# Kernel optimization log

Hardware: AMD Instinct MI355X
Metric: run time of the kernel (lower is better)

The kernel has to match this reference:

```python
import jax, jax.numpy as jnp
import numpy as np

B, S, D, H = 2, 2048, 1024, 16
DH = D // H


def setup_inputs() -> dict:
    key = jax.random.key(0)
    ks = jax.random.split(key, 12)
    sc = 1.0 / np.sqrt(D)
    return {
        "query": jax.random.normal(ks[0], (B, S, D), jnp.float32),
        "key": jax.random.normal(ks[1], (B, S, D), jnp.float32),
        "value": jax.random.normal(ks[2], (B, S, D), jnp.float32),
        "key_mask": jax.random.randint(ks[3], (B, S), 0, 2, jnp.int32),
        "Wq": jax.random.normal(ks[4], (D, D), jnp.float32) * sc,
        "bq": jnp.zeros((D,), jnp.float32),
        "Wk": jax.random.normal(ks[5], (D, D), jnp.float32) * sc,
        "bk": jnp.zeros((D,), jnp.float32),
        "Wv": jax.random.normal(ks[6], (D, D), jnp.float32) * sc,
        "bv": jnp.zeros((D,), jnp.float32),
        "Wo": jax.random.normal(ks[7], (D, D), jnp.float32) * sc,
        "bo": jnp.zeros((D,), jnp.float32),
    }


def _shape(x):
    # (B, L, D) -> (B, H, L, DH)
    return x.reshape(B, -1, H, DH).transpose(0, 2, 1, 3)


def reference(query, key, value, key_mask, Wq, bq, Wk, bk, Wv, bv, Wo, bo):
    # linear projections (torch Linear: x @ W.T + b)
    q = _shape(query @ Wq.T + bq)  # (B,H,S,DH)
    k = _shape(key @ Wk.T + bk)
    v = _shape(value @ Wv.T + bv)

    q = q / jnp.sqrt(jnp.asarray(DH, q.dtype))
    scores = jnp.einsum("bhqd,bhkd->bhqk", q, k)  # (B,H,S,S)

    pad = (key_mask == 0)[:, None, None, :]  # (B,1,1,K)
    scores = jnp.where(pad, jnp.asarray(-1e18, scores.dtype), scores)
    attn = jax.nn.softmax(scores, axis=-1)
    attn = jnp.where(pad, jnp.asarray(0.0, attn.dtype), attn)
    # dropout p=0.0 (eval) -> identity

    ctx = jnp.einsum("bhqk,bhkd->bhqd", attn, v)
    ctx = ctx.transpose(0, 2, 1, 3).reshape(B, -1, D)  # unshape
    output = ctx @ Wo.T + bo
    return (output, attn)
```

## Files before the change

### kernel.cpp

```cpp
#include <hip/hip_runtime.h>

#define B_  2
#define S_  2048
#define D_  1024
#define H_  16
#define DH_ 64

typedef _Float16 f16;
typedef f16   f16x2 __attribute__((ext_vector_type(2)));
typedef f16   f16x4 __attribute__((ext_vector_type(4)));
typedef f16   f16x8 __attribute__((ext_vector_type(8)));
typedef float f32x4 __attribute__((ext_vector_type(4)));
typedef float f32x16 __attribute__((ext_vector_type(16)));

static __device__ __forceinline__ f16x8 ldsm8(const f16* p) {
    return *reinterpret_cast<const f16x8*>(p);
}

static __device__ __forceinline__ int swz(int row, int byteInRow) {
    return row * 128 + (byteInRow ^ ((row & 7) << 4));
}

static __device__ __forceinline__ void gll16(const void* g, void* l) {
    __builtin_amdgcn_global_load_lds(
        (const __attribute__((address_space(1))) void*)g,
        (__attribute__((address_space(3))) void*)l, 16, 0, 0);
}

static __device__ __forceinline__ unsigned pk16(float a, float b) {
    return __builtin_bit_cast(unsigned, __builtin_amdgcn_cvt_pkrtz(a, b));
}

__global__ __launch_bounds__(256)
void qkv_gemm(const float* __restrict__ Aq, const float* __restrict__ Ak,
              const float* __restrict__ Av,
              const float* __restrict__ Wq, const float* __restrict__ Wk,
              const float* __restrict__ Wv,
              const float* __restrict__ bq, const float* __restrict__ bk,
              const float* __restrict__ bv,
              f16* __restrict__ qo, f16* __restrict__ ko, f16* __restrict__ vo,
              float qscale)
{
    constexpr int K = 1024, N = 1024;
    __shared__ __align__(16) f16 As[128][40];
    __shared__ __align__(16) f16 Bs[128][40];
    const int z = blockIdx.z;
    const float* A    = z == 0 ? Aq : z == 1 ? Ak : Av;
    const float* W    = z == 0 ? Wq : z == 1 ? Wk : Wv;
    const float* bias = z == 0 ? bq : z == 1 ? bk : bv;
    const float scale = z == 0 ? qscale : 1.0f;

    const int t  = threadIdx.x;
    const int bm = blockIdx.y * 128;
    const int bn = blockIdx.x * 128;
    const int w  = t >> 6, l = t & 63;
    const int wr = w >> 1, wc = w & 1;
    const int lr = l & 15, lg = l >> 4;

    f32x4 acc[4][4];
    #pragma unroll
    for (int m = 0; m < 4; ++m)
        #pragma unroll
        for (int n = 0; n < 4; ++n)
            acc[m][n] = (f32x4){0.f, 0.f, 0.f, 0.f};

    for (int kt = 0; kt < K / 32; ++kt) {
        #pragma unroll
        for (int i = 0; i < 4; ++i) {
            int idx = t + i * 256;
            int row = idx >> 3, g = idx & 7;
            float4 v = *reinterpret_cast<const float4*>(A + (size_t)(bm + row) * K + kt * 32 + g * 4);
            alignas(8) f16 hh[4] = {(f16)v.x, (f16)v.y, (f16)v.z, (f16)v.w};
            *reinterpret_cast<uint2*>(&As[row][g * 4]) = *reinterpret_cast<uint2*>(hh);
        }
        #pragma unroll
        for (int i = 0; i < 4; ++i) {
            int idx = t + i * 256;
            int row = idx >> 3, g = idx & 7;
            float4 v = *reinterpret_cast<const float4*>(W + (size_t)(bn + row) * K + kt * 32 + g * 4);
            alignas(8) f16 hh[4] = {(f16)v.x, (f16)v.y, (f16)v.z, (f16)v.w};
            *reinterpret_cast<uint2*>(&Bs[row][g * 4]) = *reinterpret_cast<uint2*>(hh);
        }
        __syncthreads();

        f16x8 af[4], bfv[4];
        #pragma unroll
        for (int m = 0; m < 4; ++m) af[m]  = ldsm8(&As[wr * 64 + m * 16 + lr][lg * 8]);
        #pragma unroll
        for (int n = 0; n < 4; ++n) bfv[n] = ldsm8(&Bs[wc * 64 + n * 16 + lr][lg * 8]);
        #pragma unroll
        for (int m = 0; m < 4; ++m)
            #pragma unroll
            for (int n = 0; n < 4; ++n)
                acc[m][n] = __builtin_amdgcn_mfma_f32_16x16x32_f16(af[m], bfv[n], acc[m][n], 0, 0, 0);
        __syncthreads();
    }

    #pragma unroll
    for (int m = 0; m < 4; ++m) {
        #pragma unroll
        for (int n = 0; n < 4; ++n) {
            int col = bn + wc * 64 + n * 16 + lr;
            float bb = bias[col];
            if (z == 2) {
                int row0 = bm + wr * 64 + m * 16 + lg * 4;
                int b = row0 >> 11, s = row0 & 2047;
                int hh_ = col >> 6, d = col & 63;
                alignas(8) f16 hv[4];
                #pragma unroll
                for (int j = 0; j < 4; ++j)
                    hv[j] = (f16)(acc[m][n][j] + bb);
                *reinterpret_cast<uint2*>(vo +
                    (((size_t)(b * 16 + hh_) * 64 + d) * 2048 + s)) =
                    *reinterpret_cast<uint2*>(hv);
            } else {
                f16* Cp = z == 0 ? qo : ko;
                #pragma unroll
                for (int j = 0; j < 4; ++j) {
                    int row = bm + wr * 64 + m * 16 + lg * 4 + j;
                    Cp[(size_t)row * N + col] = (f16)((acc[m][n][j] + bb) * scale);
                }
            }
        }
    }
}

__global__ __launch_bounds__(256)
void gemm_out(const f16* __restrict__ A, const float* __restrict__ W,
              const float* __restrict__ bias, float* __restrict__ Cp)
{
    constexpr int K = 1024, N = 1024;
    __shared__ __align__(16) f16 As[128][40];
    __shared__ __align__(16) f16 Bs[128][40];
    const int t  = threadIdx.x;
    const int bm = blockIdx.y * 128;
    const int bn = blockIdx.x * 128;
    const int w  = t >> 6, l = t & 63;
    const int wr = w >> 1, wc = w & 1;
    const int lr = l & 15, lg = l >> 4;

    f32x4 acc[4][4];
    #pragma unroll
    for (int m = 0; m < 4; ++m)
        #pragma unroll
        for (int n = 0; n < 4; ++n)
            acc[m][n] = (f32x4){0.f, 0.f, 0.f, 0.f};

    for (int kt = 0; kt < K / 32; ++kt) {
        #pragma unroll
        for (int i = 0; i < 2; ++i) {
            int idx = t + i * 256;
            int row = idx >> 2, g = idx & 3;
            *reinterpret_cast<uint4*>(&As[row][g * 8]) =
                *reinterpret_cast<const uint4*>(A + (size_t)(bm + row) * K + kt * 32 + g * 8);
        }
        #pragma unroll
        for (int i = 0; i < 4; ++i) {
            int idx = t + i * 256;
            int row = idx >> 3, g = idx & 7;
            float4 v = *reinterpret_cast<const float4*>(W + (size_t)(bn + row) * K + kt * 32 + g * 4);
            alignas(8) f16 hh[4] = {(f16)v.x, (f16)v.y, (f16)v.z, (f16)v.w};
            *reinterpret_cast<uint2*>(&Bs[row][g * 4]) = *reinterpret_cast<uint2*>(hh);
        }
        __syncthreads();

        f16x8 af[4], bfv[4];
        #pragma unroll
        for (int m = 0; m < 4; ++m) af[m]  = ldsm8(&As[wr * 64 + m * 16 + lr][lg * 8]);
        #pragma unroll
        for (int n = 0; n < 4; ++n) bfv[n] = ldsm8(&Bs[wc * 64 + n * 16 + lr][lg * 8]);
        #pragma unroll
        for (int m = 0; m < 4; ++m)
            #pragma unroll
            for (int n = 0; n < 4; ++n)
                acc[m][n] = __builtin_amdgcn_mfma_f32_16x16x32_f16(af[m], bfv[n], acc[m][n], 0, 0, 0);
        __syncthreads();
    }

    #pragma unroll
    for (int m = 0; m < 4; ++m) {
        #pragma unroll
        for (int n = 0; n < 4; ++n) {
            int col = bn + wc * 64 + n * 16 + lr;
            float bb = bias[col];
            #pragma unroll
            for (int j = 0; j < 4; ++j) {
                int row = bm + wr * 64 + m * 16 + lg * 4 + j;
                Cp[(size_t)row * N + col] = acc[m][n][j] + bb;
            }
        }
    }
}

__global__ __launch_bounds__(256, 3)
void attn_fused(const f16* __restrict__ qh, const f16* __restrict__ khp,
                const f16* __restrict__ vtg, const int* __restrict__ kmask,
                float* __restrict__ attn_out, f16* __restrict__ ch)
{
    __shared__ __align__(16) f16 ksd[2][64 * 64];
    __shared__ __align__(16) f16 vsd[2][64 * 64];
    __shared__ unsigned mbits[64];

    const int t  = threadIdx.x;
    const int w  = t >> 6, l = t & 63, lo = l & 31, hi = l >> 5;
    const bool H1 = (hi == 1);

    const int bid  = blockIdx.x;
    const int xcd  = bid & 7;
    const int slot = bid >> 3;
    const int bh   = (xcd << 2) | (slot >> 4);
    const int qt   = slot & 15;
    const int b    = bh >> 4;
    const int h    = bh & 15;
    const int q0   = qt * 128;
    const int row  = q0 + w * 32 + lo;

    f16x8 qf[4];
    {
        const f16* qb = qh + (size_t)(b * S_ + row) * D_ + h * DH_ + hi * 8;
        #pragma unroll
        for (int c = 0; c < 4; ++c) qf[c] = *reinterpret_cast<const f16x8*>(qb + c * 16);
    }

    #pragma unroll
    for (int r = 0; r < 8; ++r) {
        int ktm = w * 8 + r;
        int mkv = kmask[b * S_ + ktm * 64 + l];
        unsigned long long bl = __ballot(mkv != 0);
        if (l == 0) {
            mbits[ktm * 2]     = (unsigned)bl;
            mbits[ktm * 2 + 1] = (unsigned)(bl >> 32);
        }
    }

    const int r8 = l >> 3, l8 = l & 7;
    const int xorc8 = (l8 ^ r8) * 8;
    const f16* kgb = khp + (size_t)b * S_ * D_ + h * DH_;
    const f16* vgb = vtg + (size_t)(bh * 64) * S_;

    auto stageK = [&](int buf, int kt) {
        #pragma unroll
        for (int i = 0; i < 2; ++i) {
            int rr = i * 32 + w * 8 + r8;
            gll16(kgb + (size_t)(kt * 64 + rr) * D_ + xorc8,
                  (char*)ksd + buf * 8192 + i * 4096 + w * 1024);
        }
    };
    auto stageV = [&](int buf, int kt) {
        #pragma unroll
        for (int i = 0; i < 2; ++i) {
            int rr = i * 32 + w * 8 + r8;
            gll16(vgb + (size_t)rr * S_ + kt * 64 + xorc8,
                  (char*)vsd + buf * 8192 + i * 4096 + w * 1024);
        }
    };

    stageK(0, 0);
    __syncthreads();

    float ls = 0.f;
    int cur = 0;
    for (int kt = 0; kt < 32; ++kt) {
        if (kt + 1 < 32) stageK(cur ^ 1, kt + 1);

        f32x16 s0, s1;
        #pragma unroll
        for (int i = 0; i < 16; ++i) { s0[i] = 0.f; s1[i] = 0.f; }
        #pragma unroll
        for (int c = 0; c < 4; ++c) {
            f16x8 kf = *reinterpret_cast<const f16x8*>(
                (const char*)ksd + cur * 8192 + swz(lo, c * 32 + hi * 16));
            s0 = __builtin_amdgcn_mfma_f32_32x32x16_f16(kf, qf[c], s0, 0, 0, 0);
        }
        #pragma unroll
        for (int c = 0; c < 4; ++c) {
            f16x8 kf = *reinterpret_cast<const f16x8*>(
                (const char*)ksd + cur * 8192 + swz(lo + 32, c * 32 + hi * 16));
            s1 = __builtin_amdgcn_mfma_f32_32x32x16_f16(kf, qf[c], s1, 0, 0, 0);
        }

        const unsigned m0 = mbits[kt * 2]     >> (hi * 4);
        const unsigned m1 = mbits[kt * 2 + 1] >> (hi * 4);
        #pragma unroll
        for (int q4 = 0; q4 < 4; ++q4)
            #pragma unroll
            for (int j = 0; j < 4; ++j) {
                float e0 = __builtin_amdgcn_exp2f(s0[q4 * 4 + j]);
                float e1 = __builtin_amdgcn_exp2f(s1[q4 * 4 + j]);
                ls += ((m0 >> (q4 * 8 + j)) & 1) ? e0 : 0.0f;
                ls += ((m1 >> (q4 * 8 + j)) & 1) ? e1 : 0.0f;
            }
        __syncthreads();
        cur ^= 1;
    }

    ls += __shfl_xor(ls, 32, 64);
    const float invl = 1.0f / ls;

    stageK(0, 0);
    stageV(0, 0);
    __syncthreads();

    f32x16 oc0, oc1;
    #pragma unroll
    for (int i = 0; i < 16; ++i) { oc0[i] = 0.f; oc1[i] = 0.f; }
    cur = 0;

    float* ab = attn_out + ((size_t)bh * S_ + row) * S_ + hi * 4;

    for (int kt = 0; kt < 32; ++kt) {
        if (kt + 1 < 32) { stageK(cur ^ 1, kt + 1); stageV(cur ^ 1, kt + 1); }

        f32x16 s0, s1;
        #pragma unroll
        for (int i = 0; i < 16; ++i) { s0[i] = 0.f; s1[i] = 0.f; }
        #pragma unroll
        for (int c = 0; c < 4; ++c) {
            f16x8 kf = *reinterpret_cast<const f16x8*>(
                (const char*)ksd + cur * 8192 + swz(lo, c * 32 + hi * 16));
            s0 = __builtin_amdgcn_mfma_f32_32x32x16_f16(kf, qf[c], s0, 0, 0, 0);
        }
        #pragma unroll
        for (int c = 0; c < 4; ++c) {
            f16x8 kf = *reinterpret_cast<const f16x8*>(
                (const char*)ksd + cur * 8192 + swz(lo + 32, c * 32 + hi * 16));
            s1 = __builtin_amdgcn_mfma_f32_32x32x16_f16(kf, qf[c], s1, 0, 0, 0);
        }

        const unsigned m0 = mbits[kt * 2]     >> (hi * 4);
        const unsigned m1 = mbits[kt * 2 + 1] >> (hi * 4);
        float p0[16], p1[16];
        #pragma unroll
        for (int q4 = 0; q4 < 4; ++q4)
            #pragma unroll
            for (int j = 0; j < 4; ++j) {
                float e0 = __builtin_amdgcn_exp2f(s0[q4 * 4 + j]);
                float e1 = __builtin_amdgcn_exp2f(s1[q4 * 4 + j]);
                p0[q4 * 4 + j] = ((m0 >> (q4 * 8 + j)) & 1) ? e0 : 0.0f;
                p1[q4 * 4 + j] = ((m1 >> (q4 * 8 + j)) & 1) ? e1 : 0.0f;
            }

        #pragma unroll
        for (int q4 = 0; q4 < 4; ++q4) {
            f32x4 o0 = {p0[q4 * 4 + 0] * invl, p0[q4 * 4 + 1] * invl,
                        p0[q4 * 4 + 2] * invl, p0[q4 * 4 + 3] * invl};
            *reinterpret_cast<f32x4*>(ab + (size_t)kt * 64 + q4 * 8) = o0;
            f32x4 o1 = {p1[q4 * 4 + 0] * invl, p1[q4 * 4 + 1] * invl,
                        p1[q4 * 4 + 2] * invl, p1[q4 * 4 + 3] * invl};
            *reinterpret_cast<f32x4*>(ab + (size_t)kt * 64 + 32 + q4 * 8) = o1;
        }

        unsigned wa[2][4], wb[2][4];
        #pragma unroll
        for (int q4 = 0; q4 < 4; ++q4) {
            wa[0][q4] = pk16(p0[q4 * 4 + 0], p0[q4 * 4 + 1]);
            wb[0][q4] = pk16(p0[q4 * 4 + 2], p0[q4 * 4 + 3]);
            wa[1][q4] = pk16(p1[q4 * 4 + 0], p1[q4 * 4 + 1]);
            wb[1][q4] = pk16(p1[q4 * 4 + 2], p1[q4 * 4 + 3]);
        }

        #pragma unroll
        for (int c2 = 0; c2 < 4; ++c2) {
            const int hh = c2 >> 1, base = (c2 & 1) * 2;
            unsigned a0 = wa[hh][base], a1 = wa[hh][base + 1];
            unsigned b0 = wb[hh][base], b1 = wb[hh][base + 1];
            unsigned sa = H1 ? a0 : a1;
            unsigned sb = H1 ? b0 : b1;
            unsigned ra = (unsigned)__shfl_xor((int)sa, 32, 64);
            unsigned rb = (unsigned)__shfl_xor((int)sb, 32, 64);
            unsigned oa = H1 ? a1 : a0;
            unsigned ob = H1 ? b1 : b0;
            uint4 bw = H1 ? (uint4){ra, rb, oa, ob} : (uint4){oa, ob, ra, rb};
            f16x8 pf = __builtin_bit_cast(f16x8, bw);

            f16x8 va0 = *reinterpret_cast<const f16x8*>(
                (const char*)vsd + cur * 8192 + swz(lo, c2 * 32 + hi * 16));
            f16x8 va1 = *reinterpret_cast<const f16x8*>(
                (const char*)vsd + cur * 8192 + swz(lo + 32, c2 * 32 + hi * 16));
            oc0 = __builtin_amdgcn_mfma_f32_32x32x16_f16(va0, pf, oc0, 0, 0, 0);
            oc1 = __builtin_amdgcn_mfma_f32_32x32x16_f16(va1, pf, oc1, 0, 0, 0);
        }
        __syncthreads();
        cur ^= 1;
    }

    f16* cb = ch + (size_t)(b * S_ + row) * D_ + h * DH_;
    #pragma unroll
    for (int q4 = 0; q4 < 4; ++q4) {
        int d0 = 8 * q4 + 4 * hi;
        f16x4 v0 = {(f16)(oc0[4 * q4 + 0] * invl), (f16)(oc0[4 * q4 + 1] * invl),
                    (f16)(oc0[4 * q4 + 2] * invl), (f16)(oc0[4 * q4 + 3] * invl)};
        *reinterpret_cast<f16x4*>(cb + d0) = v0;
        f16x4 v1 = {(f16)(oc1[4 * q4 + 0] * invl), (f16)(oc1[4 * q4 + 1] * invl),
                    (f16)(oc1[4 * q4 + 2] * invl), (f16)(oc1[4 * q4 + 3] * invl)};
        *reinterpret_cast<f16x4*>(cb + 32 + d0) = v1;
    }
}

extern "C" void kernel_launch(void* const* d_in, const int* in_sizes, int n_in,
                              void* d_out, int out_size, void* d_ws, size_t ws_size,
                              hipStream_t stream) {
    const float* query = (const float*)d_in[0];
    const float* key   = (const float*)d_in[1];
    const float* value = (const float*)d_in[2];
    const int*   kmask = (const int*)d_in[3];
    const float* Wq = (const float*)d_in[4];
    const float* bq = (const float*)d_in[5];
    const float* Wk = (const float*)d_in[6];
    const float* bk = (const float*)d_in[7];
    const float* Wv = (const float*)d_in[8];
    const float* bv = (const float*)d_in[9];
    const float* Wo = (const float*)d_in[10];
    const float* bo = (const float*)d_in[11];

    float* out  = (float*)d_out;
    float* attn = out + (size_t)B_ * S_ * D_;

    const size_t NE = (size_t)B_ * S_ * D_;
    f16* qhp = (f16*)d_ws;
    f16* khp = qhp + NE;
    f16* vtg = khp + NE;
    f16* chx = vtg + NE;

    const float qscale = 0.125f * 1.44269504088896340736f;

    qkv_gemm<<<dim3(8, 32, 3), 256, 0, stream>>>(query, key, value, Wq, Wk, Wv,
                                                 bq, bk, bv, qhp, khp, vtg, qscale);

    attn_fused<<<dim3(B_ * H_ * (S_ / 128)), 256, 0, stream>>>(qhp, khp, vtg, kmask,
                                                               attn, chx);

    gemm_out<<<dim3(8, 32), 256, 0, stream>>>(chx, Wo, bo, out);
}
```

Baseline: 334.8 us.

## Triple-buffer K/V staging with explicit vmcnt waits and split softmax accumulators

Result: no change. 338.9 us (+1.2%).

```diff
diff --git a/kernel.cpp b/kernel.cpp
--- a/kernel.cpp
+++ b/kernel.cpp
@@ -197,8 +197,8 @@
                 const f16* __restrict__ vtg, const int* __restrict__ kmask,
                 float* __restrict__ attn_out, f16* __restrict__ ch)
 {
-    __shared__ __align__(16) f16 ksd[2][64 * 64];
-    __shared__ __align__(16) f16 vsd[2][64 * 64];
+    __shared__ __align__(16) f16 ksd[3][64 * 64];
+    __shared__ __align__(16) f16 vsd[3][64 * 64];
     __shared__ unsigned mbits[64];
 
     const int t  = threadIdx.x;
@@ -232,6 +232,7 @@
             mbits[ktm * 2 + 1] = (unsigned)(bl >> 32);
         }
     }
+    asm volatile("s_waitcnt vmcnt(0)" ::: "memory");
 
     const int r8 = l >> 3, l8 = l & 7;
     const int xorc8 = (l8 ^ r8) * 8;
@@ -256,12 +257,17 @@
     };
 
     stageK(0, 0);
-    __syncthreads();
-
-    float ls = 0.f;
-    int cur = 0;
+    stageK(1, 1);
+    asm volatile("s_waitcnt vmcnt(2) lgkmcnt(0)" ::: "memory");
+    __builtin_amdgcn_s_barrier();
+
+    float ls0 = 0.f, ls1 = 0.f, ls2 = 0.f, ls3 = 0.f;
     for (int kt = 0; kt < 32; ++kt) {
-        if (kt + 1 < 32) stageK(cur ^ 1, kt + 1);
+        if (kt + 2 < 32) {
+            int stg = kt + 2; int sb = stg - (stg / 3) * 3;
+            stageK(sb, stg);
+        }
+        const int cur = kt - (kt / 3) * 3;
 
         f32x16 s0, s1;
         #pragma unroll
@@ -287,29 +293,39 @@
             for (int j = 0; j < 4; ++j) {
                 float e0 = __builtin_amdgcn_exp2f(s0[q4 * 4 + j]);
                 float e1 = __builtin_amdgcn_exp2f(s1[q4 * 4 + j]);
-                ls += ((m0 >> (q4 * 8 + j)) & 1) ? e0 : 0.0f;
-                ls += ((m1 >> (q4 * 8 + j)) & 1) ? e1 : 0.0f;
+                float z0 = ((m0 >> (q4 * 8 + j)) & 1) ? e0 : 0.0f;
+                float z1 = ((m1 >> (q4 * 8 + j)) & 1) ? e1 : 0.0f;
+                if (q4 < 2) { ls0 += z0; ls2 += z1; }
+                else        { ls1 += z0; ls3 += z1; }
             }
-        __syncthreads();
-        cur ^= 1;
-    }
-
+
+        if (kt < 30)      asm volatile("s_waitcnt vmcnt(2)" ::: "memory");
+        else if (kt == 30) asm volatile("s_waitcnt vmcnt(0)" ::: "memory");
+        else               asm volatile("s_waitcnt vmcnt(0) lgkmcnt(0)" ::: "memory");
+        __builtin_amdgcn_s_barrier();
+    }
+
+    float ls = (ls0 + ls1) + (ls2 + ls3);
     ls += __shfl_xor(ls, 32, 64);
     const float invl = 1.0f / ls;
 
-    stageK(0, 0);
-    stageV(0, 0);
-    __syncthreads();
+    stageK(0, 0); stageV(0, 0);
+    stageK(1, 1); stageV(1, 1);
+    asm volatile("s_waitcnt vmcnt(4)" ::: "memory");
+    __builtin_amdgcn_s_barrier();
 
     f32x16 oc0, oc1;
     #pragma unroll
     for (int i = 0; i < 16; ++i) { oc0[i] = 0.f; oc1[i] = 0.f; }
-    cur = 0;
 
     float* ab = attn_out + ((size_t)bh * S_ + row) * S_ + hi * 4;
 
     for (int kt = 0; kt < 32; ++kt) {
-        if (kt + 1 < 32) { stageK(cur ^ 1, kt + 1); stageV(cur ^ 1, kt + 1); }
+        if (kt + 2 < 32) {
+            int stg = kt + 2; int sb = stg - (stg / 3) * 3;
+            stageK(sb, stg); stageV(sb, stg);
+        }
+        const int cur = kt - (kt / 3) * 3;
 
         f32x16 s0, s1;
         #pragma unroll
@@ -358,16 +374,15 @@
             wa[1][q4] = pk16(p1[q4 * 4 + 0], p1[q4 * 4 + 1]);
             wb[1][q4] = pk16(p1[q4 * 4 + 2], p1[q4 * 4 + 3]);
         }
-
         #pragma unroll
         for (int c2 = 0; c2 < 4; ++c2) {
             const int hh = c2 >> 1, base = (c2 & 1) * 2;
             unsigned a0 = wa[hh][base], a1 = wa[hh][base + 1];
             unsigned b0 = wb[hh][base], b1 = wb[hh][base + 1];
             unsigned sa = H1 ? a0 : a1;
-            unsigned sb = H1 ? b0 : b1;
+            unsigned sb2 = H1 ? b0 : b1;
             unsigned ra = (unsigned)__shfl_xor((int)sa, 32, 64);
-            unsigned rb = (unsigned)__shfl_xor((int)sb, 32, 64);
+            unsigned rb = (unsigned)__shfl_xor((int)sb2, 32, 64);
             unsigned oa = H1 ? a1 : a0;
             unsigned ob = H1 ? b1 : b0;
             uint4 bw = H1 ? (uint4){ra, rb, oa, ob} : (uint4){oa, ob, ra, rb};
@@ -380,8 +395,11 @@
             oc0 = __builtin_amdgcn_mfma_f32_32x32x16_f16(va0, pf, oc0, 0, 0, 0);
             oc1 = __builtin_amdgcn_mfma_f32_32x32x16_f16(va1, pf, oc1, 0, 0, 0);
         }
-        __syncthreads();
-        cur ^= 1;
+
+        if (kt == 0)       asm volatile("s_waitcnt vmcnt(12)" ::: "memory");
+        else if (kt < 30)  asm volatile("s_waitcnt vmcnt(20)" ::: "memory");
+        else if (kt == 30) asm volatile("s_waitcnt vmcnt(16)" ::: "memory");
+        if (kt < 31) __builtin_amdgcn_s_barrier();
     }
 
     f16* cb = ch + (size_t)(b * S_ + row) * D_ + h * DH_;
```

## Split score tiles into halves, raise occupancy, use explicit waitcnt barriers

Applied to the files above, without the earlier changes.

Result: faster. 328.2 us (-2.0%).

```diff
diff --git a/kernel.cpp b/kernel.cpp
--- a/kernel.cpp
+++ b/kernel.cpp
@@ -192,7 +192,7 @@
     }
 }
 
-__global__ __launch_bounds__(256, 3)
+__global__ __launch_bounds__(256, 4)
 void attn_fused(const f16* __restrict__ qh, const f16* __restrict__ khp,
                 const f16* __restrict__ vtg, const int* __restrict__ kmask,
                 float* __restrict__ attn_out, f16* __restrict__ ch)
@@ -232,6 +232,7 @@
             mbits[ktm * 2 + 1] = (unsigned)(bl >> 32);
         }
     }
+    asm volatile("s_waitcnt vmcnt(0)" ::: "memory");
 
     const int r8 = l >> 3, l8 = l & 7;
     const int xorc8 = (l8 ^ r8) * 8;
@@ -256,132 +257,122 @@
     };
 
     stageK(0, 0);
-    __syncthreads();
-
-    float ls = 0.f;
-    int cur = 0;
+    asm volatile("s_waitcnt vmcnt(0) lgkmcnt(0)" ::: "memory");
+    __builtin_amdgcn_s_barrier();
+
+    float ls0 = 0.f, ls1 = 0.f;
     for (int kt = 0; kt < 32; ++kt) {
-        if (kt + 1 < 32) stageK(cur ^ 1, kt + 1);
-
-        f32x16 s0, s1;
-        #pragma unroll
-        for (int i = 0; i < 16; ++i) { s0[i] = 0.f; s1[i] = 0.f; }
-        #pragma unroll
-        for (int c = 0; c < 4; ++c) {
-            f16x8 kf = *reinterpret_cast<const f16x8*>(
-                (const char*)ksd + cur * 8192 + swz(lo, c * 32 + hi * 16));
-            s0 = __builtin_amdgcn_mfma_f32_32x32x16_f16(kf, qf[c], s0, 0, 0, 0);
-        }
-        #pragma unroll
-        for (int c = 0; c < 4; ++c) {
-            f16x8 kf = *reinterpret_cast<const f16x8*>(
-                (const char*)ksd + cur * 8192 + swz(lo + 32, c * 32 + hi * 16));
-            s1 = __builtin_amdgcn_mfma_f32_32x32x16_f16(kf, qf[c], s1, 0, 0, 0);
-        }
-
-        const unsigned m0 = mbits[kt * 2]     >> (hi * 4);
-        const unsigned m1 = mbits[kt * 2 + 1] >> (hi * 4);
-        #pragma unroll
-        for (int q4 = 0; q4 < 4; ++q4)
-            #pragma unroll
-            for (int j = 0; j < 4; ++j) {
-                float e0 = __builtin_amdgcn_exp2f(s0[q4 * 4 + j]);
-                float e1 = __builtin_amdgcn_exp2f(s1[q4 * 4 + j]);
-                ls += ((m0 >> (q4 * 8 + j)) & 1) ? e0 : 0.0f;
-                ls += ((m1 >> (q4 * 8 + j)) & 1) ? e1 : 0.0f;
-            }
-        __syncthreads();
-        cur ^= 1;
-    }
-
+        if (kt + 1 < 32) stageK((kt + 1) & 1, kt + 1);
+        const int cur = kt & 1;
+
+        #pragma unroll
+        for (int h2 = 0; h2 < 2; ++h2) {
+            f32x16 s;
+            #pragma unroll
+            for (int i = 0; i < 16; ++i) s[i] = 0.f;
+            #pragma unroll
+            for (int c = 0; c < 4; ++c) {
+                f16x8 kf = *reinterpret_cast<const f16x8*>(
+                    (const char*)ksd + cur * 8192 + swz(lo + h2 * 32, c * 32 + hi * 16));
+                s = __builtin_amdgcn_mfma_f32_32x32x16_f16(kf, qf[c], s, 0, 0, 0);
+            }
+            const unsigned m = mbits[kt * 2 + h2] >> (hi * 4);
+            #pragma unroll
+            for (int q4 = 0; q4 < 4; ++q4)
+                #pragma unroll
+                for (int j = 0; j < 4; ++j) {
+                    float e = __builtin_amdgcn_exp2f(s[q4 * 4 + j]);
+                    float z = ((m >> (q4 * 8 + j)) & 1) ? e : 0.0f;
+                    if (q4 & 1) ls1 += z; else ls0 += z;
+                }
+        }
+        asm volatile("s_waitcnt vmcnt(0)" ::: "memory");
+        __builtin_amdgcn_s_barrier();
+    }
+
+    float ls = ls0 + ls1;
     ls += __shfl_xor(ls, 32, 64);
     const float invl = 1.0f / ls;
 
-    stageK(0, 0);
-    stageV(0, 0);
-    __syncthreads();
+    stageK(0, 0); stageV(0, 0);
+    asm volatile("s_waitcnt vmcnt(0)" ::: "memory");
+    __builtin_amdgcn_s_barrier();
 
     f32x16 oc0, oc1;
     #pragma unroll
     for (int i = 0; i < 16; ++i) { oc0[i] = 0.f; oc1[i] = 0.f; }
-    cur = 0;
 
     float* ab = attn_out + ((size_t)bh * S_ + row) * S_ + hi * 4;
 
     for (int kt = 0; kt < 32; ++kt) {
-        if (kt + 1 < 32) { stageK(cur ^ 1, kt + 1); stageV(cur ^ 1, kt + 1); }
-
-        f32x16 s0, s1;
-        #pragma unroll
-        for (int i = 0; i < 16; ++i) { s0[i] = 0.f; s1[i] = 0.f; }
-        #pragma unroll
-        for (int c = 0; c < 4; ++c) {
-            f16x8 kf = *reinterpret_cast<const f16x8*>(
-                (const char*)ksd + cur * 8192 + swz(lo, c * 32 + hi * 16));
-            s0 = __builtin_amdgcn_mfma_f32_32x32x16_f16(kf, qf[c], s0, 0, 0, 0);
-        }
-        #pragma unroll
-        for (int c = 0; c < 4; ++c) {
-            f16x8 kf = *reinterpret_cast<const f16x8*>(
-                (const char*)ksd + cur * 8192 + swz(lo + 32, c * 32 + hi * 16));
-            s1 = __builtin_amdgcn_mfma_f32_32x32x16_f16(kf, qf[c], s1, 0, 0, 0);
-        }
-
-        const unsigned m0 = mbits[kt * 2]     >> (hi * 4);
-        const unsigned m1 = mbits[kt * 2 + 1] >> (hi * 4);
-        float p0[16], p1[16];
-        #pragma unroll
-        for (int q4 = 0; q4 < 4; ++q4)
-            #pragma unroll
-            for (int j = 0; j < 4; ++j) {
-                float e0 = __builtin_amdgcn_exp2f(s0[q4 * 4 + j]);
-                float e1 = __builtin_amdgcn_exp2f(s1[q4 * 4 + j]);
-                p0[q4 * 4 + j] = ((m0 >> (q4 * 8 + j)) & 1) ? e0 : 0.0f;
-                p1[q4 * 4 + j] = ((m1 >> (q4 * 8 + j)) & 1) ? e1 : 0.0f;
-            }
-
-        #pragma unroll
-        for (int q4 = 0; q4 < 4; ++q4) {
-            f32x4 o0 = {p0[q4 * 4 + 0] * invl, p0[q4 * 4 + 1] * invl,
-                        p0[q4 * 4 + 2] * invl, p0[q4 * 4 + 3] * invl};
-            *reinterpret_cast<f32x4*>(ab + (size_t)kt * 64 + q4 * 8) = o0;
-            f32x4 o1 = {p1[q4 * 4 + 0] * invl, p1[q4 * 4 + 1] * invl,
-                        p1[q4 * 4 + 2] * invl, p1[q4 * 4 + 3] * invl};
-            *reinterpret_cast<f32x4*>(ab + (size_t)kt * 64 + 32 + q4 * 8) = o1;
-        }
-
-        unsigned wa[2][4], wb[2][4];
-        #pragma unroll
-        for (int q4 = 0; q4 < 4; ++q4) {
-            wa[0][q4] = pk16(p0[q4 * 4 + 0], p0[q4 * 4 + 1]);
-            wb[0][q4] = pk16(p0[q4 * 4 + 2], p0[q4 * 4 + 3]);
-            wa[1][q4] = pk16(p1[q4 * 4 + 0], p1[q4 * 4 + 1]);
-            wb[1][q4] = pk16(p1[q4 * 4 + 2], p1[q4 * 4 + 3]);
-        }
-
-        #pragma unroll
-        for (int c2 = 0; c2 < 4; ++c2) {
-            const int hh = c2 >> 1, base = (c2 & 1) * 2;
-            unsigned a0 = wa[hh][base], a1 = wa[hh][base + 1];
-            unsigned b0 = wb[hh][base], b1 = wb[hh][base + 1];
-            unsigned sa = H1 ? a0 : a1;
-            unsigned sb = H1 ? b0 : b1;
-            unsigned ra = (unsigned)__shfl_xor((int)sa, 32, 64);
-            unsigned rb = (unsigned)__shfl_xor((int)sb, 32, 64);
-            unsigned oa = H1 ? a1 : a0;
-            unsigned ob = H1 ? b1 : b0;
-            uint4 bw = H1 ? (uint4){ra, rb, oa, ob} : (uint4){oa, ob, ra, rb};
-            f16x8 pf = __builtin_bit_cast(f16x8, bw);
-
-            f16x8 va0 = *reinterpret_cast<const f16x8*>(
-                (const char*)vsd + cur * 8192 + swz(lo, c2 * 32 + hi * 16));
-            f16x8 va1 = *reinterpret_cast<const f16x8*>(
-                (const char*)vsd + cur * 8192 + swz(lo + 32, c2 * 32 + hi * 16));
-            oc0 = __builtin_amdgcn_mfma_f32_32x32x16_f16(va0, pf, oc0, 0, 0, 0);
-            oc1 = __builtin_amdgcn_mfma_f32_32x32x16_f16(va1, pf, oc1, 0, 0, 0);
-        }
-        __syncthreads();
-        cur ^= 1;
+        if (kt + 1 < 32) {
+            stageK((kt + 1) & 1, kt + 1);
+            stageV((kt + 1) & 1, kt + 1);
+        }
+        const int cur = kt & 1;
+
+        #pragma unroll
+        for (int h2 = 0; h2 < 2; ++h2) {
+            f32x16 s;
+            #pragma unroll
+            for (int i = 0; i < 16; ++i) s[i] = 0.f;
+            #pragma unroll
+            for (int c = 0; c < 4; ++c) {
+                f16x8 kf = *reinterpret_cast<const f16x8*>(
+                    (const char*)ksd + cur * 8192 + swz(lo + h2 * 32, c * 32 + hi * 16));
+                s = __builtin_amdgcn_mfma_f32_32x32x16_f16(kf, qf[c], s, 0, 0, 0);
+            }
+
+            const unsigned m = mbits[kt * 2 + h2] >> (hi * 4);
+            float p[16];
+            #pragma unroll
+            for (int q4 = 0; q4 < 4; ++q4)
+                #pragma unroll
+                for (int j = 0; j < 4; ++j) {
+                    float e = __builtin_amdgcn_exp2f(s[q4 * 4 + j]);
+                    p[q4 * 4 + j] = ((m >> (q4 * 8 + j)) & 1) ? e : 0.0f;
+                }
+
+            #pragma unroll
+            for (int q4 = 0; q4 < 4; ++q4) {
+                f32x4 o = {p[q4 * 4 + 0] * invl, p[q4 * 4 + 1] * invl,
+                           p[q4 * 4 + 2] * invl, p[q4 * 4 + 3] * invl};
+                *reinterpret_cast<f32x4*>(ab + (size_t)kt * 64 + h2 * 32 + q4 * 8) = o;
+            }
+
+            unsigned wa4[4], wb4[4];
+            #pragma unroll
+            for (int q4 = 0; q4 < 4; ++q4) {
+                wa4[q4] = pk16(p[q4 * 4 + 0], p[q4 * 4 + 1]);
+                wb4[q4] = pk16(p[q4 * 4 + 2], p[q4 * 4 + 3]);
+            }
+            #pragma unroll
+            for (int cc = 0; cc < 2; ++cc) {
+                const int c2 = h2 * 2 + cc, base = cc * 2;
+                unsigned a0 = wa4[base], a1 = wa4[base + 1];
+                unsigned b0 = wb4[base], b1 = wb4[base + 1];
+                unsigned sa = H1 ? a0 : a1;
+                unsigned sb = H1 ? b0 : b1;
+                unsigned ra = (unsigned)__shfl_xor((int)sa, 32, 64);
+                unsigned rb = (unsigned)__shfl_xor((int)sb, 32, 64);
+                unsigned oa = H1 ? a1 : a0;
+                unsigned ob = H1 ? b1 : b0;
+                uint4 bw = H1 ? (uint4){ra, rb, oa, ob} : (uint4){oa, ob, ra, rb};
+                f16x8 pf = __builtin_bit_cast(f16x8, bw);
+
+                f16x8 va0 = *reinterpret_cast<const f16x8*>(
+                    (const char*)vsd + cur * 8192 + swz(lo, c2 * 32 + hi * 16));
+                f16x8 va1 = *reinterpret_cast<const f16x8*>(
+                    (const char*)vsd + cur * 8192 + swz(lo + 32, c2 * 32 + hi * 16));
+                oc0 = __builtin_amdgcn_mfma_f32_32x32x16_f16(va0, pf, oc0, 0, 0, 0);
+                oc1 = __builtin_amdgcn_mfma_f32_32x32x16_f16(va1, pf, oc1, 0, 0, 0);
+            }
+        }
+
+        if (kt < 31) {
+            asm volatile("s_waitcnt vmcnt(8)" ::: "memory");
+            __builtin_amdgcn_s_barrier();
+        }
     }
 
     f16* cb = ch + (size_t)(b * S_ + row) * D_ + h * DH_;
```
